# Performance work log

Measured on AMD Instinct MI355X. Metric: run time of the kernel, lower is better.

The kernel has to match this reference:

```python
import jax, jax.numpy as jnp
import numpy as np

B, M = 4, 8192
NUM_PAD = 1024  # trailing pc columns zeroed to exercise the zero-column mask


def setup_inputs() -> dict:
    key = jax.random.key(0)
    k1, k2 = jax.random.split(key)
    vertices = jax.random.normal(k1, (B, 3, 128, 64), dtype=jnp.float32)
    pc = jax.random.normal(k2, (B, 3, M), dtype=jnp.float32)
    # zero-pad some columns: the original filters columns where all 3 coords == 0
    pc = pc.at[:, :, M - NUM_PAD:].set(0.0)
    return {"vertices": vertices, "pc": pc}


def reference(vertices, pc):
    b = vertices.shape[0]
    v = vertices.reshape(b, 3, -1).transpose(0, 2, 1)   # [B, N, 3] mesh vertices
    p = pc.transpose(0, 2, 1)                           # [B, M, 3] point cloud
    valid = ~jnp.all(pc == 0.0, axis=1)                 # [B, M] non-zero columns
    # squared pairwise distances pc -> vertices: [B, M, N]
    d2 = (
        jnp.sum(p * p, axis=-1)[:, :, None]
        + jnp.sum(v * v, axis=-1)[:, None, :]
        - 2.0 * jnp.einsum("bmd,bnd->bmn", p, v)
    )
    dist2 = jnp.min(d2, axis=-1)                        # [B, M] NN sq-dist per pc point
    valid_f = valid.astype(dist2.dtype)
    per_item = jnp.sum(dist2 * valid_f, axis=-1) / jnp.sum(valid_f, axis=-1)  # mean over valid points
    return jnp.mean(per_item)
```

## Files before the change

kernel.cpp:

```cpp
#include <hip/hip_runtime.h>

typedef float v2f    __attribute__((ext_vector_type(2)));
typedef float f32x16 __attribute__((ext_vector_type(16)));
typedef short short8 __attribute__((ext_vector_type(8)));

#define MPTS 8192
#define NVERT 8192
#define NTILE (NVERT/32)
#define NCHUNK 2
#define TPB 256

static __device__ __forceinline__ unsigned short bhi(float f) {
    return (unsigned short)(__float_as_uint(f) >> 16);
}
static __device__ __forceinline__ float bf2f(unsigned short h) {
    return __uint_as_float(((unsigned int)h) << 16);
}

__global__ __launch_bounds__(TPB) void prep_kernel(
        const float* __restrict__ vert,
        unsigned short* __restrict__ bfrag)
{
    const int idx = blockIdx.x * TPB + threadIdx.x;
    const int b = idx >> 13, v = idx & (NVERT - 1);
    const float* vb = vert + (size_t)b * 3 * NVERT;
    const float x = vb[v], y = vb[v + NVERT], z = vb[v + 2 * NVERT];
    const unsigned short hx = bhi(x), hy = bhi(y), hz = bhi(z);
    const unsigned short lx = bhi(x - bf2f(hx));
    const unsigned short ly = bhi(y - bf2f(hy));
    const unsigned short lz = bhi(z - bf2f(hz));
    const float w = fmaf(x, x, fmaf(y, y, z * z));
    const unsigned short hw = bhi(w);
    const unsigned short lw = bhi(w - bf2f(hw));

    const int tile = v >> 5, c = v & 31;
    unsigned short* base = bfrag + ((size_t)b * NTILE + tile) * 512;
    short8 g0 = {(short)hx, (short)hy, (short)hz,
                 (short)hx, (short)hy, (short)hz, (short)lx, (short)ly};
    short8 g1 = {(short)lz, (short)hw, (short)lw, 0, 0, 0, 0, 0};
    *(short8*)(base + c * 8)        = g0;
    *(short8*)(base + (c + 32) * 8) = g1;
}

__global__ __launch_bounds__(TPB, 2) void minpart_kernel(
        const unsigned short* __restrict__ bfrag,
        const float* __restrict__ pc,
        float* __restrict__ partial)
{
    const int b = blockIdx.z, chunk = blockIdx.y;
    const int tid = threadIdx.x;
    const int wave = tid >> 6, l = tid & 63;
    const int half = l >> 5, lm = l & 31;
    const int strip = blockIdx.x * 4 + wave;
    const int pm = strip * 32 + lm;

    const float* pcb = pc + (size_t)b * 3 * MPTS;
    const float ax = -2.0f * pcb[pm];
    const float ay = -2.0f * pcb[pm + MPTS];
    const float az = -2.0f * pcb[pm + 2 * MPTS];
    const unsigned short hx = bhi(ax), hy = bhi(ay), hz = bhi(az);
    const unsigned short lx = bhi(ax - bf2f(hx));
    const unsigned short ly = bhi(ay - bf2f(hy));
    const unsigned short lz = bhi(az - bf2f(hz));
    const unsigned short ONE = 0x3F80;

    short8 A;
    A[0] = half ? (short)hz : (short)hx;
    A[1] = half ? (short)ONE : (short)hy;
    A[2] = half ? (short)ONE : (short)hz;
    A[3] = half ? (short)0   : (short)lx;
    A[4] = half ? (short)0   : (short)ly;
    A[5] = half ? (short)0   : (short)lz;
    A[6] = half ? (short)0   : (short)hx;
    A[7] = half ? (short)0   : (short)hy;

    const unsigned short* bp =
        bfrag + ((size_t)b * NTILE + chunk * (NTILE / NCHUNK)) * 512 + l * 8;

    f32x16 run;
    #pragma unroll
    for (int i = 0; i < 16; ++i) run[i] = 1e30f;
    const f32x16 zero = {};

    #pragma unroll 4
    for (int j = 0; j < NTILE / NCHUNK; ++j) {
        const short8 bv = *(const short8*)(bp + (size_t)j * 512);
        const f32x16 d = __builtin_amdgcn_mfma_f32_32x32x16_bf16(A, bv, zero, 0, 0, 0);
        #pragma unroll
        for (int i = 0; i < 16; ++i) run[i] = fminf(run[i], d[i]);
    }

    #pragma unroll
    for (int m = 16; m; m >>= 1) {
        #pragma unroll
        for (int i = 0; i < 16; ++i)
            run[i] = fminf(run[i], __shfl_xor(run[i], m));
    }

    if (lm == 0) {
        float* po = partial + ((size_t)b * NCHUNK + chunk) * MPTS + strip * 32;
        #pragma unroll
        for (int r = 0; r < 16; ++r)
            po[(r & 3) + 8 * (r >> 2) + 4 * half] = run[r];
    }
}

__global__ __launch_bounds__(64) void reduce_kernel(
        const float* __restrict__ pc,
        const float* __restrict__ partial,
        v2f* __restrict__ part)
{
    const int b = blockIdx.x >> 5, sl = blockIdx.x & 31;
    const int tid = threadIdx.x;
    const int m = sl * 256 + tid * 4;
    const float* pcb = pc + (size_t)b * 3 * MPTS;
    const float* pb  = partial + (size_t)b * NCHUNK * MPTS;

    float4 t = *(const float4*)(pb + m);
    #pragma unroll
    for (int c = 1; c < NCHUNK; ++c) {
        const float4 u = *(const float4*)(pb + (size_t)c * MPTS + m);
        t.x = fminf(t.x, u.x); t.y = fminf(t.y, u.y);
        t.z = fminf(t.z, u.z); t.w = fminf(t.w, u.w);
    }
    const float4 x = *(const float4*)(pcb + m);
    const float4 y = *(const float4*)(pcb + MPTS + m);
    const float4 z = *(const float4*)(pcb + 2 * MPTS + m);

    float sum = 0.0f, cnt = 0.0f;
    {
        const float xs[4] = {x.x, x.y, x.z, x.w};
        const float ys[4] = {y.x, y.y, y.z, y.w};
        const float zs[4] = {z.x, z.y, z.z, z.w};
        const float ts[4] = {t.x, t.y, t.z, t.w};
        #pragma unroll
        for (int i = 0; i < 4; ++i) {
            const float d2 = fmaf(xs[i], xs[i], fmaf(ys[i], ys[i],
                             fmaf(zs[i], zs[i], ts[i])));
            if (!(xs[i] == 0.0f && ys[i] == 0.0f && zs[i] == 0.0f)) {
                sum += d2; cnt += 1.0f;
            }
        }
    }
    #pragma unroll
    for (int off = 32; off; off >>= 1) {
        sum += __shfl_down(sum, off);
        cnt += __shfl_down(cnt, off);
    }
    if (tid == 0) part[blockIdx.x] = (v2f){sum, cnt};
}

__global__ __launch_bounds__(128) void final_kernel(
        const v2f* __restrict__ part, float* __restrict__ out, int B)
{
    __shared__ float ss[128], sc[128];
    const int t = threadIdx.x;
    v2f p = (v2f){0.0f, 0.0f};
    if (t < B * 32) p = part[t];
    ss[t] = p.x; sc[t] = p.y;
    __syncthreads();
    if (t == 0) {
        float acc = 0.0f;
        for (int b = 0; b < B; ++b) {
            float s = 0.0f, c = 0.0f;
            for (int i = 0; i < 32; ++i) { s += ss[b * 32 + i]; c += sc[b * 32 + i]; }
            acc += s / c;
        }
        out[0] = acc / (float)B;
    }
}

extern "C" void kernel_launch(void* const* d_in, const int* in_sizes, int n_in,
                              void* d_out, int out_size, void* d_ws, size_t ws_size,
                              hipStream_t stream) {
    const float* vert = (const float*)d_in[0];
    const float* pc   = (const float*)d_in[1];
    float* out        = (float*)d_out;
    const int B = in_sizes[0] / (3 * NVERT);

    unsigned short* bfrag = (unsigned short*)d_ws;
    float* partial = (float*)((char*)d_ws + (size_t)B * NTILE * 512 * sizeof(unsigned short));
    v2f* part = (v2f*)(partial + (size_t)B * NCHUNK * MPTS);

    prep_kernel<<<B * NVERT / TPB, TPB, 0, stream>>>(vert, bfrag);
    dim3 grid(NVERT / 32 / 4, NCHUNK, B);
    minpart_kernel<<<grid, TPB, 0, stream>>>(bfrag, pc, partial);
    reduce_kernel<<<B * 32, 64, 0, stream>>>(pc, partial, part);
    final_kernel<<<1, 128, 0, stream>>>(part, out, B);
}
```

Baseline: 84.25 us.

## Swap MFMA operand roles, register-block four point strips per wave

```diff
diff --git a/kernel.cpp b/kernel.cpp
--- a/kernel.cpp
+++ b/kernel.cpp
@@ -7,7 +7,9 @@
 #define MPTS 8192
 #define NVERT 8192
 #define NTILE (NVERT/32)
-#define NCHUNK 2
+#define NCHUNK 16
+#define TPC (NTILE/NCHUNK)
+#define NSTRIP 4
 #define TPB 256
 
 static __device__ __forceinline__ unsigned short bhi(float f) {
@@ -19,7 +21,7 @@
 
 __global__ __launch_bounds__(TPB) void prep_kernel(
         const float* __restrict__ vert,
-        unsigned short* __restrict__ bfrag)
+        unsigned short* __restrict__ afrag)
 {
     const int idx = blockIdx.x * TPB + threadIdx.x;
     const int b = idx >> 13, v = idx & (NVERT - 1);
@@ -34,7 +36,7 @@
     const unsigned short lw = bhi(w - bf2f(hw));
 
     const int tile = v >> 5, c = v & 31;
-    unsigned short* base = bfrag + ((size_t)b * NTILE + tile) * 512;
+    unsigned short* base = afrag + ((size_t)b * NTILE + tile) * 512;
     short8 g0 = {(short)hx, (short)hy, (short)hz,
                  (short)hx, (short)hy, (short)hz, (short)lx, (short)ly};
     short8 g1 = {(short)lz, (short)hw, (short)lw, 0, 0, 0, 0, 0};
@@ -42,8 +44,8 @@
     *(short8*)(base + (c + 32) * 8) = g1;
 }
 
-__global__ __launch_bounds__(TPB, 2) void minpart_kernel(
-        const unsigned short* __restrict__ bfrag,
+__global__ __launch_bounds__(TPB, 4) void minpart_kernel(
+        const unsigned short* __restrict__ afrag,
         const float* __restrict__ pc,
         float* __restrict__ partial)
 {
@@ -51,57 +53,63 @@
     const int tid = threadIdx.x;
     const int wave = tid >> 6, l = tid & 63;
     const int half = l >> 5, lm = l & 31;
-    const int strip = blockIdx.x * 4 + wave;
-    const int pm = strip * 32 + lm;
+    const int group = blockIdx.x * 4 + wave;
+    const unsigned short ONE = 0x3F80;
 
     const float* pcb = pc + (size_t)b * 3 * MPTS;
-    const float ax = -2.0f * pcb[pm];
-    const float ay = -2.0f * pcb[pm + MPTS];
-    const float az = -2.0f * pcb[pm + 2 * MPTS];
-    const unsigned short hx = bhi(ax), hy = bhi(ay), hz = bhi(az);
-    const unsigned short lx = bhi(ax - bf2f(hx));
-    const unsigned short ly = bhi(ay - bf2f(hy));
-    const unsigned short lz = bhi(az - bf2f(hz));
-    const unsigned short ONE = 0x3F80;
+    short8 Bf[NSTRIP];
+    #pragma unroll
+    for (int q = 0; q < NSTRIP; ++q) {
+        const int pm = group * 128 + q * 32 + lm;
+        const float ax = -2.0f * pcb[pm];
+        const float ay = -2.0f * pcb[pm + MPTS];
+        const float az = -2.0f * pcb[pm + 2 * MPTS];
+        const unsigned short hx = bhi(ax), hy = bhi(ay), hz = bhi(az);
+        const unsigned short lx = bhi(ax - bf2f(hx));
+        const unsigned short ly = bhi(ay - bf2f(hy));
+        const unsigned short lz = bhi(az - bf2f(hz));
+        Bf[q][0] = half ? (short)hz : (short)hx;
+        Bf[q][1] = half ? (short)ONE : (short)hy;
+        Bf[q][2] = half ? (short)ONE : (short)hz;
+        Bf[q][3] = half ? (short)0   : (short)lx;
+        Bf[q][4] = half ? (short)0   : (short)ly;
+        Bf[q][5] = half ? (short)0   : (short)lz;
+        Bf[q][6] = half ? (short)0   : (short)hx;
+        Bf[q][7] = half ? (short)0   : (short)hy;
+    }
 
-    short8 A;
-    A[0] = half ? (short)hz : (short)hx;
-    A[1] = half ? (short)ONE : (short)hy;
-    A[2] = half ? (short)ONE : (short)hz;
-    A[3] = half ? (short)0   : (short)lx;
-    A[4] = half ? (short)0   : (short)ly;
-    A[5] = half ? (short)0   : (short)lz;
-    A[6] = half ? (short)0   : (short)hx;
-    A[7] = half ? (short)0   : (short)hy;
+    const unsigned short* ap =
+        afrag + ((size_t)b * NTILE + chunk * TPC) * 512 + l * 8;
 
-    const unsigned short* bp =
-        bfrag + ((size_t)b * NTILE + chunk * (NTILE / NCHUNK)) * 512 + l * 8;
-
-    f32x16 run;
+    f32x16 run[NSTRIP];
     #pragma unroll
-    for (int i = 0; i < 16; ++i) run[i] = 1e30f;
+    for (int q = 0; q < NSTRIP; ++q)
+        #pragma unroll
+        for (int i = 0; i < 16; ++i) run[q][i] = 1e30f;
     const f32x16 zero = {};
 
-    #pragma unroll 4
-    for (int j = 0; j < NTILE / NCHUNK; ++j) {
-        const short8 bv = *(const short8*)(bp + (size_t)j * 512);
-        const f32x16 d = __builtin_amdgcn_mfma_f32_32x32x16_bf16(A, bv, zero, 0, 0, 0);
+    #pragma unroll 2
+    for (int j = 0; j < TPC; ++j) {
+        const short8 Av = *(const short8*)(ap + (size_t)j * 512);
         #pragma unroll
-        for (int i = 0; i < 16; ++i) run[i] = fminf(run[i], d[i]);
+        for (int q = 0; q < NSTRIP; ++q) {
+            const f32x16 d = __builtin_amdgcn_mfma_f32_32x32x16_bf16(Av, Bf[q], zero, 0, 0, 0);
+            #pragma unroll
+            for (int i = 0; i < 16; ++i) run[q][i] = fminf(run[q][i], d[i]);
+        }
     }
 
+    float* po = partial + ((size_t)b * NCHUNK + chunk) * MPTS + group * 128;
     #pragma unroll
-    for (int m = 16; m; m >>= 1) {
-        #pragma unroll
-        for (int i = 0; i < 16; ++i)
-            run[i] = fminf(run[i], __shfl_xor(run[i], m));
-    }
-
-    if (lm == 0) {
-        float* po = partial + ((size_t)b * NCHUNK + chunk) * MPTS + strip * 32;
-        #pragma unroll
-        for (int r = 0; r < 16; ++r)
-            po[(r & 3) + 8 * (r >> 2) + 4 * half] = run[r];
+    for (int q = 0; q < NSTRIP; ++q) {
+        float m01 = fminf(run[q][0], run[q][1]), m23 = fminf(run[q][2], run[q][3]);
+        float m45 = fminf(run[q][4], run[q][5]), m67 = fminf(run[q][6], run[q][7]);
+        float m89 = fminf(run[q][8], run[q][9]), mab = fminf(run[q][10], run[q][11]);
+        float mcd = fminf(run[q][12], run[q][13]), mef = fminf(run[q][14], run[q][15]);
+        float m = fminf(fminf(fminf(m01, m23), fminf(m45, m67)),
+                        fminf(fminf(m89, mab), fminf(mcd, mef)));
+        m = fminf(m, __shfl_xor(m, 32));
+        if (half == 0) po[q * 32 + lm] = m;
     }
 }
 
@@ -178,13 +186,13 @@
     float* out        = (float*)d_out;
     const int B = in_sizes[0] / (3 * NVERT);
 
-    unsigned short* bfrag = (unsigned short*)d_ws;
+    unsigned short* afrag = (unsigned short*)d_ws;
     float* partial = (float*)((char*)d_ws + (size_t)B * NTILE * 512 * sizeof(unsigned short));
     v2f* part = (v2f*)(partial + (size_t)B * NCHUNK * MPTS);
 
-    prep_kernel<<<B * NVERT / TPB, TPB, 0, stream>>>(vert, bfrag);
-    dim3 grid(NVERT / 32 / 4, NCHUNK, B);
-    minpart_kernel<<<grid, TPB, 0, stream>>>(bfrag, pc, partial);
+    prep_kernel<<<B * NVERT / TPB, TPB, 0, stream>>>(vert, afrag);
+    dim3 grid(64 / NSTRIP, NCHUNK, B);
+    minpart_kernel<<<grid, TPB, 0, stream>>>(afrag, pc, partial);
     reduce_kernel<<<B * 32, 64, 0, stream>>>(pc, partial, part);
     final_kernel<<<1, 128, 0, stream>>>(part, out, B);
 }
```

New measurement: 79.82 us. -5.3%, faster.
